# Kernel tuning notes

Measured on AMD Instinct MI355X. Metric: run time of the kernel, lower is better.

## Reference

```python
import jax, jax.numpy as jnp
import numpy as np

K_TOP = 16
TEMP = 1.0
EPS = 1e-9

def setup_inputs() -> dict:
    key = jax.random.key(0)
    k1, k2, k3 = jax.random.split(key, 3)
    B, H, N, D = 4, 8, 2048, 64
    q = jax.random.normal(k1, (B, H, N, D), dtype=jnp.float32)
    k = jax.random.normal(k2, (B, H, N, D), dtype=jnp.float32)
    u = jax.random.uniform(k3, (B, N, N), dtype=jnp.float32)
    return {"q": q, "k": k, "u": u}

def reference(q, k, u):
    # q, k: [B, H, N, D]; u: uniform noise [B, N, N]
    d_head = q.shape[-1]
    scale = 1.0 / jnp.sqrt(jnp.asarray(d_head, dtype=q.dtype))
    # [B, H, N, N] scores, then mean over heads -> [B, N, N]
    attn_scores = jnp.einsum('bhnd,bhmd->bhnm', q, k) * scale
    logits = attn_scores.mean(axis=1)
    gumbel = -jnp.log(-jnp.log(u + EPS) + EPS)
    probs = jax.nn.softmax((logits + gumbel) / TEMP, axis=-1)
    topk_vals = jax.lax.top_k(probs, K_TOP)[0]          # [B, N, K]
    thresh = topk_vals.min(axis=-1, keepdims=True)      # [B, N, 1]
    sparse_mask = (probs >= thresh).astype(probs.dtype)
    return sparse_mask[:, None, :, :]                   # [B, 1, N, N]
```

## Files before the change

kernel.cpp:

```cpp
#include <hip/hip_runtime.h>
#include <math.h>

#define BB 4
#define HH 8
#define NN 2048
#define DD 64
#define KTOP 16
#define CUT_MARGIN 1e-3f

typedef _Float16 half_t;
typedef __attribute__((ext_vector_type(8))) _Float16 half8;
typedef __attribute__((ext_vector_type(4))) float floatx4;

__device__ __forceinline__ void gl_lds16(const half_t* g, half_t* l) {
    __builtin_amdgcn_global_load_lds(
        (const __attribute__((address_space(1))) void*)g,
        (__attribute__((address_space(3))) void*)l, 16, 0, 0);
}

__global__ __launch_bounds__(256) void split_swz(const float* __restrict__ q,
                                                 const float* __restrict__ kk,
                                                 half_t* __restrict__ qhi,
                                                 half_t* __restrict__ qlo,
                                                 half_t* __restrict__ khi,
                                                 half_t* __restrict__ klo) {
    const int uidx = blockIdx.x * 256 + threadIdx.x;
    const size_t src = (size_t)uidx * 8;
    const int R   = uidx >> 3;
    const int kg8 = uidx & 7;
    const int bh  = R >> 11;
    const int n   = R & 2047;
    const int kb  = kg8 >> 2;
    const int kgw = kg8 & 3;
    const int tile = n >> 7;
    const int r    = n & 127;
    const int p    = ((r >> 3) << 5) + (kgw << 3) + (r & 7);
    const size_t dst = (((size_t)(bh * 2 + kb) * 16 + tile) * 512 + p) * 8;

    float a[8], b[8];
    *(float4*)&a[0] = *(const float4*)(q + src);
    *(float4*)&a[4] = *(const float4*)(q + src + 4);
    *(float4*)&b[0] = *(const float4*)(kk + src);
    *(float4*)&b[4] = *(const float4*)(kk + src + 4);
    half8 qh, ql, kh, kl;
#pragma unroll
    for (int e = 0; e < 8; ++e) {
        half_t hq = (half_t)a[e];
        half_t hk = (half_t)b[e];
        qh[e] = hq; ql[e] = (half_t)((a[e] - (float)hq) * 2048.0f);
        kh[e] = hk; kl[e] = (half_t)((b[e] - (float)hk) * 2048.0f);
    }
    *(half8*)(qhi + dst) = qh;
    *(half8*)(qlo + dst) = ql;
    *(half8*)(khi + dst) = kh;
    *(half8*)(klo + dst) = kl;
}

__global__ __launch_bounds__(256, 2) void gemm_f16x3(const half_t* __restrict__ qhi,
                                                     const half_t* __restrict__ qlo,
                                                     const half_t* __restrict__ khi,
                                                     const half_t* __restrict__ klo,
                                                     float* __restrict__ L) {
    const int b  = blockIdx.z;
    const int i0 = blockIdx.y * 128;
    const int j0 = blockIdx.x * 128;
    const int tid  = threadIdx.x;
    const int wave = __builtin_amdgcn_readfirstlane(tid >> 6);
    const int lane = tid & 63;
    const int wr = wave >> 1, wc = wave & 1;
    const int lm = lane & 15, quad = lane >> 4;

    __shared__ __align__(16) half_t Ah[2][4096];
    __shared__ __align__(16) half_t Al[2][4096];
    __shared__ __align__(16) half_t Bh[2][4096];
    __shared__ __align__(16) half_t Bl[2][4096];

    const half_t* gmat;
    half_t* lmat;
    int tileoff;
    if      (wave == 0) { gmat = qhi; lmat = &Ah[0][0]; tileoff = (i0 >> 7) * 4096; }
    else if (wave == 1) { gmat = qlo; lmat = &Al[0][0]; tileoff = (i0 >> 7) * 4096; }
    else if (wave == 2) { gmat = khi; lmat = &Bh[0][0]; tileoff = (j0 >> 7) * 4096; }
    else                { gmat = klo; lmat = &Bl[0][0]; tileoff = (j0 >> 7) * 4096; }
    const half_t* glane0 = gmat + (size_t)(b * 16) * 65536 + tileoff + lane * 8;

#define STAGE(sv, bufv)                                                       \
    {                                                                         \
        const half_t* gs = glane0 + (size_t)(sv) * 65536;                     \
        half_t* ls = lmat + (bufv) * 4096;                                    \
        _Pragma("unroll") for (int i = 0; i < 8; ++i)                         \
            gl_lds16(gs + i * 512, ls + i * 512);                             \
    }

#define LOADFRAG(bufv)                                                        \
    _Pragma("unroll") for (int t = 0; t < 4; ++t) {                           \
        const int am = wr * 64 + t * 16 + lm;                                 \
        const int bm = wc * 64 + t * 16 + lm;                                 \
        const int ai = ((am >> 3) << 8) + (quad << 6) + ((am & 7) << 3);      \
        const int bi = ((bm >> 3) << 8) + (quad << 6) + ((bm & 7) << 3);      \
        fah[t] = *(const half8*)&Ah[bufv][ai];                                \
        fal[t] = *(const half8*)&Al[bufv][ai];                                \
        fbh[t] = *(const half8*)&Bh[bufv][bi];                                \
        fbl[t] = *(const half8*)&Bl[bufv][bi];                                \
    }

#define MFMAS                                                                 \
    {                                                                         \
        __builtin_amdgcn_s_setprio(1);                                        \
        _Pragma("unroll") for (int tr = 0; tr < 4; ++tr)                      \
            _Pragma("unroll") for (int tc = 0; tc < 4; ++tc) {                \
                acc1[tr][tc] = __builtin_amdgcn_mfma_f32_16x16x32_f16(        \
                    fah[tr], fbh[tc], acc1[tr][tc], 0, 0, 0);                 \
                acc2[tr][tc] = __builtin_amdgcn_mfma_f32_16x16x32_f16(        \
                    fah[tr], fbl[tc], acc2[tr][tc], 0, 0, 0);                 \
                acc2[tr][tc] = __builtin_amdgcn_mfma_f32_16x16x32_f16(        \
                    fal[tr], fbh[tc], acc2[tr][tc], 0, 0, 0);                 \
            }                                                                 \
        __builtin_amdgcn_s_setprio(0);                                        \
    }

#define WAITL0 { asm volatile("s_waitcnt lgkmcnt(0)" ::: "memory");           \
                 __builtin_amdgcn_sched_barrier(0); }
#define WAITV8 { asm volatile("s_waitcnt vmcnt(8)" ::: "memory");             \
                 __builtin_amdgcn_sched_barrier(0); }
#define WAITV0 { asm volatile("s_waitcnt vmcnt(0)" ::: "memory");             \
                 __builtin_amdgcn_sched_barrier(0); }
#define BAR    { __builtin_amdgcn_s_barrier();                                \
                 __builtin_amdgcn_sched_barrier(0); }

    floatx4 acc1[4][4], acc2[4][4];
#pragma unroll
    for (int tr = 0; tr < 4; ++tr)
#pragma unroll
        for (int tc = 0; tc < 4; ++tc) {
            acc1[tr][tc] = (floatx4)0.0f;
            acc2[tr][tc] = (floatx4)0.0f;
        }

    half8 fah[4], fal[4], fbh[4], fbl[4];

    STAGE(0, 0);
    STAGE(1, 1);
    WAITV8;
    BAR;

#pragma unroll 2
    for (int s = 0; s < 14; ++s) {
        const int cur = s & 1;
        LOADFRAG(cur);
        WAITL0;
        BAR;
        STAGE(s + 2, cur);
        MFMAS;
        WAITV8;
        BAR;
    }
    LOADFRAG(0);
    WAITL0;
    BAR;
    MFMAS;
    WAITV0;
    BAR;
    LOADFRAG(1);
    WAITL0;
    MFMAS;

#undef STAGE
#undef LOADFRAG
#undef MFMAS
#undef WAITL0
#undef WAITV8
#undef WAITV0
#undef BAR

    const float s1 = 0.015625f;
    const float s2 = 0.015625f / 2048.0f;
#pragma unroll
    for (int tr = 0; tr < 4; ++tr)
#pragma unroll
        for (int r = 0; r < 4; ++r) {
            const int grow = i0 + wr * 64 + tr * 16 + quad * 4 + r;
            float* Lp = L + ((size_t)b * NN + grow) * NN + j0 + wc * 64 + lm;
#pragma unroll
            for (int tc = 0; tc < 4; ++tc)
                Lp[tc * 16] = acc1[tr][tc][r] * s1 + acc2[tr][tc][r] * s2;
        }
}

__device__ __forceinline__ unsigned long long flip64(double x) {
    unsigned long long v = (unsigned long long)__double_as_longlong(x);
    return v ^ ((0ULL - (v >> 63)) | 0x8000000000000000ULL);
}
__device__ __forceinline__ double unflip64(unsigned long long k) {
    unsigned long long v = (k >> 63) ? (k ^ 0x8000000000000000ULL) : ~k;
    return __longlong_as_double((long long)v);
}

__global__ __launch_bounds__(256) void topk_mask(float* __restrict__ LM,
                                                 const float* __restrict__ u) {
    const int wave = threadIdx.x >> 6;
    const int lane = threadIdx.x & 63;
    const int row  = blockIdx.x * 4 + wave;
    float* lrow = LM + (size_t)row * NN;
    const float* urow = u + (size_t)row * NN;

    __shared__ int s_idx[4][64];

    float z[32];
    unsigned hard = 0;
    float4 lb = *(const float4*)(lrow + lane * 4);
    float4 ub = *(const float4*)(urow + lane * 4);
#pragma unroll
    for (int e = 0; e < 8; ++e) {
        float4 lnx, unx;
        if (e < 7) {
            lnx = *(const float4*)(lrow + (e + 1) * 256 + lane * 4);
            unx = *(const float4*)(urow + (e + 1) * 256 + lane * 4);
        }
        const float* ls = (const float*)&lb;
        const float* us = (const float*)&ub;
#pragma unroll
        for (int s = 0; s < 4; ++s) {
            float w = -__logf(us[s] + 1e-9f);
            z[e * 4 + s] = ls[s] - __logf(w + 1e-9f);
            hard |= (us[s] > 0.999f ? 1u : 0u) << (e * 4 + s);
        }
        lb = lnx; ub = unx;
    }

    float v = z[0];
#pragma unroll
    for (int r = 1; r < 32; ++r) v = fmaxf(v, z[r]);
#pragma unroll
    for (int kS = 2; kS <= 64; kS <<= 1) {
#pragma unroll
        for (int j = kS >> 1; j > 0; j >>= 1) {
            float o = __shfl_xor(v, j, 64);
            bool asc = ((lane & kS) == 0);
            bool lower = ((lane & j) == 0);
            float mn = fminf(v, o), mx = fmaxf(v, o);
            v = (asc == lower) ? mn : mx;
        }
    }
    const float cut = __shfl(v, 48, 64) - CUT_MARGIN;

    int c = 0;
#pragma unroll
    for (int r = 0; r < 32; ++r) {
        bool p = (z[r] >= cut);
        unsigned long long m = __ballot(p);
        if (p) {
            int slot = c + __popcll(m & ((1ULL << lane) - 1ULL));
            if (slot < 64) s_idx[wave][slot] = (r >> 2) * 256 + lane * 4 + (r & 3);
        }
        c += __popcll(m);
    }
    if (c > 64) c = 64;

    unsigned long long key = 0xFFFFFFFFFFFFFFFFULL;
    if (lane < c) {
        int idx = s_idx[wave][lane];
        double uu = (double)urow[idx] + 1e-9;
        double w  = -log(uu);
        double g  = -log(w + 1e-9);
        key = flip64((double)lrow[idx] + g);
    }
#pragma unroll
    for (int kS = 2; kS <= 64; kS <<= 1) {
#pragma unroll
        for (int j = kS >> 1; j > 0; j >>= 1) {
            unsigned long long o = __shfl_xor(key, j, 64);
            bool asc = ((lane & kS) == 0);
            bool lower = ((lane & j) == 0);
            unsigned long long mn = (key < o) ? key : o;
            unsigned long long mx = (key < o) ? o : key;
            key = (asc == lower) ? mn : mx;
        }
    }
    const double thresh = unflip64(__shfl(key, c - KTOP, 64));

    const float t_hi = (float)thresh + 3e-4f;
    const float t_lo = (float)thresh - 3e-4f;
    unsigned bm = hard;
#pragma unroll
    for (int r = 0; r < 32; ++r)
        bm |= ((z[r] <= t_hi && z[r] >= t_lo) ? 1u : 0u) << r;
    while (bm) {
        int t = __builtin_ctz(bm);
        bm &= bm - 1;
        const int idx = (t >> 2) * 256 + lane * 4 + (t & 3);
        double uu = (double)urow[idx] + 1e-9;
        double w  = -log(uu);
        double g  = -log(w + 1e-9);
        double z64 = (double)lrow[idx] + g;
        z[t] = (z64 >= thresh) ? 1.0e30f : -1.0e30f;
    }

#pragma unroll
    for (int e = 0; e < 8; ++e) {
        float o[4];
#pragma unroll
        for (int s = 0; s < 4; ++s)
            o[s] = (z[e * 4 + s] > t_hi) ? 1.0f : 0.0f;
        *(float4*)(lrow + e * 256 + lane * 4) = *(float4*)o;
    }
}

extern "C" void kernel_launch(void* const* d_in, const int* in_sizes, int n_in,
                              void* d_out, int out_size, void* d_ws, size_t ws_size,
                              hipStream_t stream) {
    const float* q = (const float*)d_in[0];
    const float* k = (const float*)d_in[1];
    const float* u = (const float*)d_in[2];
    float* out = (float*)d_out;
    const size_t NQ = (size_t)BB * HH * NN * DD;
    half_t* qhi = (half_t*)d_ws;
    half_t* qlo = qhi + NQ;
    half_t* khi = qlo + NQ;
    half_t* klo = khi + NQ;

    split_swz<<<(int)(NQ / 8 / 256), 256, 0, stream>>>(q, k, qhi, qlo, khi, klo);

    dim3 grid1(NN / 128, NN / 128, BB);
    gemm_f16x3<<<grid1, 256, 0, stream>>>(qhi, qlo, khi, klo, out);

    topk_mask<<<BB * NN / 4, 256, 0, stream>>>(out, u);
}
```

Baseline: 218.3 us.

## Enlarge GEMM tile to 256x128 with 8 waves and triple-buffered LDS pipeline

```diff
diff --git a/kernel.cpp b/kernel.cpp
--- a/kernel.cpp
+++ b/kernel.cpp
@@ -56,13 +56,13 @@
     *(half8*)(klo + dst) = kl;
 }
 
-__global__ __launch_bounds__(256, 2) void gemm_f16x3(const half_t* __restrict__ qhi,
+__global__ __launch_bounds__(512, 2) void gemm_f16x3(const half_t* __restrict__ qhi,
                                                      const half_t* __restrict__ qlo,
                                                      const half_t* __restrict__ khi,
                                                      const half_t* __restrict__ klo,
                                                      float* __restrict__ L) {
     const int b  = blockIdx.z;
-    const int i0 = blockIdx.y * 128;
+    const int i0 = blockIdx.y * 256;
     const int j0 = blockIdx.x * 128;
     const int tid  = threadIdx.x;
     const int wave = __builtin_amdgcn_readfirstlane(tid >> 6);
@@ -70,64 +70,61 @@
     const int wr = wave >> 1, wc = wave & 1;
     const int lm = lane & 15, quad = lane >> 4;
 
-    __shared__ __align__(16) half_t Ah[2][4096];
-    __shared__ __align__(16) half_t Al[2][4096];
-    __shared__ __align__(16) half_t Bh[2][4096];
-    __shared__ __align__(16) half_t Bl[2][4096];
-
-    const half_t* gmat;
-    half_t* lmat;
-    int tileoff;
-    if      (wave == 0) { gmat = qhi; lmat = &Ah[0][0]; tileoff = (i0 >> 7) * 4096; }
-    else if (wave == 1) { gmat = qlo; lmat = &Al[0][0]; tileoff = (i0 >> 7) * 4096; }
-    else if (wave == 2) { gmat = khi; lmat = &Bh[0][0]; tileoff = (j0 >> 7) * 4096; }
-    else                { gmat = klo; lmat = &Bl[0][0]; tileoff = (j0 >> 7) * 4096; }
-    const half_t* glane0 = gmat + (size_t)(b * 16) * 65536 + tileoff + lane * 8;
-
-#define STAGE(sv, bufv)                                                       \
-    {                                                                         \
-        const half_t* gs = glane0 + (size_t)(sv) * 65536;                     \
-        half_t* ls = lmat + (bufv) * 4096;                                    \
-        _Pragma("unroll") for (int i = 0; i < 8; ++i)                         \
-            gl_lds16(gs + i * 512, ls + i * 512);                             \
-    }
-
-#define LOADFRAG(bufv)                                                        \
-    _Pragma("unroll") for (int t = 0; t < 4; ++t) {                           \
-        const int am = wr * 64 + t * 16 + lm;                                 \
-        const int bm = wc * 64 + t * 16 + lm;                                 \
-        const int ai = ((am >> 3) << 8) + (quad << 6) + ((am & 7) << 3);      \
-        const int bi = ((bm >> 3) << 8) + (quad << 6) + ((bm & 7) << 3);      \
-        fah[t] = *(const half8*)&Ah[bufv][ai];                                \
-        fal[t] = *(const half8*)&Al[bufv][ai];                                \
-        fbh[t] = *(const half8*)&Bh[bufv][bi];                                \
-        fbl[t] = *(const half8*)&Bl[bufv][bi];                                \
-    }
-
-#define MFMAS                                                                 \
-    {                                                                         \
-        __builtin_amdgcn_s_setprio(1);                                        \
-        _Pragma("unroll") for (int tr = 0; tr < 4; ++tr)                      \
-            _Pragma("unroll") for (int tc = 0; tc < 4; ++tc) {                \
-                acc1[tr][tc] = __builtin_amdgcn_mfma_f32_16x16x32_f16(        \
-                    fah[tr], fbh[tc], acc1[tr][tc], 0, 0, 0);                 \
-                acc2[tr][tc] = __builtin_amdgcn_mfma_f32_16x16x32_f16(        \
-                    fah[tr], fbl[tc], acc2[tr][tc], 0, 0, 0);                 \
-                acc2[tr][tc] = __builtin_amdgcn_mfma_f32_16x16x32_f16(        \
-                    fal[tr], fbh[tc], acc2[tr][tc], 0, 0, 0);                 \
-            }                                                                 \
-        __builtin_amdgcn_s_setprio(0);                                        \
-    }
+    __shared__ __align__(16) half_t lds[3 * 24576];
+
+    int aidx[4], bidx[4];
+#pragma unroll
+    for (int t = 0; t < 4; ++t) {
+        const int am = wr * 64 + t * 16 + lm;
+        const int bm = wc * 64 + t * 16 + lm;
+        aidx[t] = ((am >> 3) << 8) + (quad << 6) + ((am & 7) << 3);
+        bidx[t] = 16384 + ((bm >> 3) << 8) + (quad << 6) + ((bm & 7) << 3);
+    }
+
+    const size_t tileA = (size_t)(i0 >> 7) * 4096;
+    const size_t tileB = (size_t)(j0 >> 7) * 4096;
+    const size_t bbase = (size_t)(b * 16) * 65536;
+    const half_t* gq[6];
+    int lq[6];
+#pragma unroll
+    for (int q = 0; q < 6; ++q) {
+        const int c = wave * 6 + q;
+        const half_t* base;
+        size_t off;
+        if (c < 16)      { base = qhi; off = tileA + (size_t)c * 512; }
+        else if (c < 32) { base = qlo; off = tileA + (size_t)(c - 16) * 512; }
+        else if (c < 40) { base = khi; off = tileB + (size_t)(c - 32) * 512; }
+        else             { base = klo; off = tileB + (size_t)(c - 40) * 512; }
+        gq[q] = base + bbase + off + lane * 8;
+        lq[q] = c * 512;
+    }
+
+#define ISSUE(q_, s_, nb_)                                                    \
+    gl_lds16(gq[q_] + (size_t)(s_) * 65536, &lds[(nb_) * 24576 + lq[q_]])
 
 #define WAITL0 { asm volatile("s_waitcnt lgkmcnt(0)" ::: "memory");           \
                  __builtin_amdgcn_sched_barrier(0); }
-#define WAITV8 { asm volatile("s_waitcnt vmcnt(8)" ::: "memory");             \
+#define WAITV6 { asm volatile("s_waitcnt vmcnt(6)" ::: "memory");             \
                  __builtin_amdgcn_sched_barrier(0); }
 #define WAITV0 { asm volatile("s_waitcnt vmcnt(0)" ::: "memory");             \
                  __builtin_amdgcn_sched_barrier(0); }
 #define BAR    { __builtin_amdgcn_s_barrier();                                \
                  __builtin_amdgcn_sched_barrier(0); }
 
+#define MF(tr_)                                                               \
+    {                                                                         \
+        __builtin_amdgcn_s_setprio(1);                                        \
+        _Pragma("unroll") for (int tc = 0; tc < 4; ++tc) {                    \
+            acc1[tr_][tc] = __builtin_amdgcn_mfma_f32_16x16x32_f16(           \
+                ah, bh[tc], acc1[tr_][tc], 0, 0, 0);                          \
+            acc2[tr_][tc] = __builtin_amdgcn_mfma_f32_16x16x32_f16(           \
+                ah, bl[tc], acc2[tr_][tc], 0, 0, 0);                          \
+            acc2[tr_][tc] = __builtin_amdgcn_mfma_f32_16x16x32_f16(           \
+                al, bh[tc], acc2[tr_][tc], 0, 0, 0);                          \
+        }                                                                     \
+        __builtin_amdgcn_s_setprio(0);                                        \
+    }
+
     floatx4 acc1[4][4], acc2[4][4];
 #pragma unroll
     for (int tr = 0; tr < 4; ++tr)
@@ -137,41 +134,57 @@
             acc2[tr][tc] = (floatx4)0.0f;
         }
 
-    half8 fah[4], fal[4], fbh[4], fbl[4];
-
-    STAGE(0, 0);
-    STAGE(1, 1);
-    WAITV8;
+#pragma unroll
+    for (int q = 0; q < 6; ++q) ISSUE(q, 0, 0);
+#pragma unroll
+    for (int q = 0; q < 6; ++q) ISSUE(q, 1, 1);
+    WAITV6;
     BAR;
 
-#pragma unroll 2
-    for (int s = 0; s < 14; ++s) {
-        const int cur = s & 1;
-        LOADFRAG(cur);
-        WAITL0;
+#pragma unroll
+    for (int s = 0; s < 16; ++s) {
+        const int bb = (s % 3) * 24576;
+        const int nb = (s + 2) % 3;
+        half8 bh[4], bl[4], ah, al;
+#pragma unroll
+        for (int t = 0; t < 4; ++t) {
+            bh[t] = *(const half8*)&lds[bb + bidx[t]];
+            bl[t] = *(const half8*)&lds[bb + 4096 + bidx[t]];
+        }
+        ah = *(const half8*)&lds[bb + aidx[0]];
+        al = *(const half8*)&lds[bb + 8192 + aidx[0]];
+        if (s < 14) { ISSUE(0, s + 2, nb); ISSUE(1, s + 2, nb); }
+        BAR; WAITL0;
+        MF(0);
         BAR;
-        STAGE(s + 2, cur);
-        MFMAS;
-        WAITV8;
+        ah = *(const half8*)&lds[bb + aidx[1]];
+        al = *(const half8*)&lds[bb + 8192 + aidx[1]];
+        if (s < 14) { ISSUE(2, s + 2, nb); ISSUE(3, s + 2, nb); }
+        BAR; WAITL0;
+        MF(1);
         BAR;
-    }
-    LOADFRAG(0);
-    WAITL0;
-    BAR;
-    MFMAS;
-    WAITV0;
-    BAR;
-    LOADFRAG(1);
-    WAITL0;
-    MFMAS;
-
-#undef STAGE
-#undef LOADFRAG
-#undef MFMAS
+        ah = *(const half8*)&lds[bb + aidx[2]];
+        al = *(const half8*)&lds[bb + 8192 + aidx[2]];
+        if (s < 14) { ISSUE(4, s + 2, nb); }
+        BAR; WAITL0;
+        MF(2);
+        BAR;
+        ah = *(const half8*)&lds[bb + aidx[3]];
+        al = *(const half8*)&lds[bb + 8192 + aidx[3]];
+        if (s < 14) { ISSUE(5, s + 2, nb); }
+        if (s < 14) { WAITV6; }
+        else if (s == 14) { WAITV0; }
+        BAR; WAITL0;
+        MF(3);
+        if (s < 15) BAR;
+    }
+
+#undef ISSUE
 #undef WAITL0
-#undef WAITV8
+#undef WAITV6
 #undef WAITV0
 #undef BAR
+#undef MF
 
     const float s1 = 0.015625f;
     const float s2 = 0.015625f / 2048.0f;
@@ -321,8 +334,8 @@
 
     split_swz<<<(int)(NQ / 8 / 256), 256, 0, stream>>>(q, k, qhi, qlo, khi, klo);
 
-    dim3 grid1(NN / 128, NN / 128, BB);
-    gemm_f16x3<<<grid1, 256, 0, stream>>>(qhi, qlo, khi, klo, out);
+    dim3 grid1(NN / 128, NN / 256, BB);
+    gemm_f16x3<<<grid1, 512, 0, stream>>>(qhi, qlo, khi, klo, out);
 
     topk_mask<<<BB * NN / 4, 256, 0, stream>>>(out, u);
 }
```

After: 221.3 us. About the same (+1.3%).
